# Kernel tuning notes

Hardware: AMD Instinct MI355X
Metric: run time of the kernel (lower is better)

The kernel has to match this reference:

```python
import jax, jax.numpy as jnp
import numpy as np

N = 50000
E = 400000
IN_NODE = 256
IN_EATTR = 64
IN_ETYPE = 64
EMB_EATTR = 128
EMB_ETYPE = 128
EMB_NODE = 128
OUT = 128
HEADS = 8
N_NODE_TYPES = 3
SLOPE = 0.2


def _lrelu(x):
    return jnp.where(x >= 0, x, SLOPE * x)


def setup_inputs() -> dict:
    key = jax.random.key(0)
    ks = jax.random.split(key, 12)
    s = lambda fan_in: 1.0 / np.sqrt(fan_in)
    return {
        "node_feats": jax.random.normal(ks[0], (N, IN_NODE), dtype=jnp.float32),
        "edge_index": jax.random.randint(ks[1], (2, E), 0, N, dtype=jnp.int64),
        "edge_attr": jax.random.normal(ks[2], (E, IN_EATTR), dtype=jnp.float32),
        "edge_type": jax.random.normal(ks[3], (E, IN_ETYPE), dtype=jnp.float32),
        "node_type_list": jax.random.randint(ks[4], (N,), 0, N_NODE_TYPES, dtype=jnp.int64),
        "edge_type_list": jax.random.randint(ks[5], (E,), 0, 4, dtype=jnp.int64),
        # one Linear per node type, stacked: [T, in, emb]
        "W_node": jax.random.uniform(ks[6], (N_NODE_TYPES, IN_NODE, EMB_NODE), jnp.float32, -s(IN_NODE), s(IN_NODE)),
        "W_eattr": jax.random.uniform(ks[7], (IN_EATTR, EMB_EATTR), jnp.float32, -s(IN_EATTR), s(IN_EATTR)),
        "W_etype": jax.random.uniform(ks[8], (IN_ETYPE, EMB_ETYPE), jnp.float32, -s(IN_ETYPE), s(IN_ETYPE)),
        "W_upd": jax.random.uniform(ks[9], (EMB_NODE + EMB_EATTR, OUT), jnp.float32, -s(EMB_NODE + EMB_EATTR), s(EMB_NODE + EMB_EATTR)),
        "W_attn": jax.random.uniform(ks[10], (EMB_EATTR + EMB_ETYPE + 2 * EMB_NODE, HEADS), jnp.float32, -s(512), s(512)),
    }


def reference(node_feats, edge_index, edge_attr, edge_type, node_type_list,
              edge_type_list, W_node, W_eattr, W_etype, W_upd, W_attn):
    # type-specific node embedding: project with all type weights, select per node
    all_emb = jnp.einsum("ni,tio->tno", node_feats, W_node)            # [T, N, emb]
    node_emb = jnp.take_along_axis(all_emb, node_type_list[None, :, None], axis=0)[0]  # [N, emb]

    attr_emb = _lrelu(edge_attr @ W_eattr)                             # [E, emb_a]
    type_emb = _lrelu(edge_type @ W_etype)                             # [E, emb_t]

    src, tar = edge_index[0], edge_index[1]
    src_emb = node_emb[src]                                            # [E, emb]
    tar_emb = node_emb[tar]                                            # [E, emb]

    # cat(tar_emb, attr_emb, type_emb, src_emb) -> attention scores per edge
    feat = jnp.concatenate([tar_emb, attr_emb, type_emb, src_emb], axis=1)
    scores = _lrelu(feat @ W_attn)                                     # [E, H]

    # segment softmax over edges grouped by SOURCE node (torch softmax(dim=1)
    # on the dense [src, tar, H] matrix; -10000 fillers underflow to 0)
    seg_max = jax.ops.segment_max(scores, src, num_segments=N)         # [N, H]
    ex = jnp.exp(scores - seg_max[src])
    denom = jax.ops.segment_sum(ex, src, num_segments=N)               # [N, H]
    attn = ex / denom[src]                                             # [E, H]

    msg = _lrelu(jnp.concatenate([src_emb, attr_emb], axis=1) @ W_upd) # [E, O]
    out = jax.ops.segment_sum(attn[:, :, None] * msg[:, None, :], src, num_segments=N)  # [N, H, O]
    return out.reshape(N, HEADS * OUT)
```

## Files before the change

kernel.cpp:

```cpp
#include <hip/hip_runtime.h>
#include <hip/hip_bf16.h>

#define N_NODES 50000
#define N_EDGES 400000
#define SLOPE 0.2f

typedef __attribute__((ext_vector_type(8))) short bf16x8;
typedef __attribute__((ext_vector_type(4))) float f32x4;
#define MFMA_BF16 __builtin_amdgcn_mfma_f32_16x16x32_bf16

static __device__ __forceinline__ float lrelu(float x) { return x >= 0.f ? x : SLOPE * x; }
static __device__ __forceinline__ float b2f(__hip_bfloat16 x) { return __bfloat162float(x); }
static __device__ __forceinline__ float u2f(unsigned short u) {
    union { unsigned short u; __hip_bfloat16 b; } cv; cv.u = u; return __bfloat162float(cv.b);
}
static __device__ __forceinline__ unsigned short f2bf(float x) {
    union { __hip_bfloat16 b; unsigned short u; } cv; cv.b = __float2bfloat16(x); return cv.u;
}
static __device__ __forceinline__ int clampi(int v, int lo, int hi) {
    return v < lo ? lo : (v > hi ? hi : v);
}
static __device__ __forceinline__ float ldF(const void* __restrict__ p, size_t i, bool isb) {
    return isb ? b2f(((const __hip_bfloat16*)p)[i]) : ((const float*)p)[i];
}
static __device__ __forceinline__ int ldI(const void* __restrict__ p, size_t i, bool i64) {
    return i64 ? (int)(((const long long*)p)[i]) : ((const int*)p)[i];
}

__global__ void k_detect(const void* __restrict__ nf, const void* __restrict__ eidx,
                         int* __restrict__ flags)
{
    int t = threadIdx.x;
    float x = b2f(((const __hip_bfloat16*)nf)[2 * t]);
    bool bad = !(x == x) || fabsf(x) > 1e4f;
    unsigned long long fmask = __ballot(bad);
    int v = ((const int*)eidx)[2 * t + 1];
    unsigned long long imask = __ballot(v != 0);
    if (t == 0) {
        flags[0] = (fmask == 0ull) ? 1 : 0;
        flags[1] = (imask == 0ull) ? 1 : 0;
    }
}

__global__ __launch_bounds__(256) void k_wprep(
    const void* __restrict__ Wn, const void* __restrict__ Wea, const void* __restrict__ Wet,
    const void* __restrict__ Wup, const void* __restrict__ Wat,
    unsigned short* __restrict__ WnT, unsigned short* __restrict__ WeaT,
    unsigned short* __restrict__ WetT, unsigned short* __restrict__ Wu1T,
    unsigned short* __restrict__ Wu2T, unsigned short* __restrict__ WatMidT,
    unsigned short* __restrict__ WatTS, const int* __restrict__ flags)
{
    const bool isb = flags[0] != 0;
    int i = blockIdx.x * 256 + threadIdx.x;
    if (i < 3 * 128 * 256) {
        int ty = i >> 15, rem = i & 32767, c = rem >> 8, k = rem & 255;
        WnT[i] = f2bf(ldF(Wn, ((size_t)ty * 256 + k) * 128 + c, isb));
    }
    if (i < 128 * 128) {
        int c = i >> 7, k = i & 127;
        Wu1T[i] = f2bf(ldF(Wup, (size_t)k * 128 + c, isb));
        Wu2T[i] = f2bf(ldF(Wup, (size_t)(128 + k) * 128 + c, isb));
    }
    if (i < 128 * 64) {
        int c = i >> 6, k = i & 63;
        WeaT[i] = f2bf(ldF(Wea, (size_t)k * 128 + c, isb));
        WetT[i] = f2bf(ldF(Wet, (size_t)k * 128 + c, isb));
    }
    if (i < 16 * 256) {
        int c = i >> 8, k = i & 255;
        WatMidT[i] = (c < 8) ? f2bf(ldF(Wat, (size_t)(128 + k) * 8 + c, isb)) : (unsigned short)0;
    }
    if (i < 16 * 128) {
        int c = i >> 7, k = i & 127;
        WatTS[i] = (c < 8) ? f2bf(ldF(Wat, (size_t)k * 8 + c, isb))
                           : f2bf(ldF(Wat, (size_t)(384 + k) * 8 + (c - 8), isb));
    }
}

__global__ __launch_bounds__(256) void k_node(
    const void* __restrict__ nf, const void* __restrict__ ntype,
    const unsigned short* __restrict__ WnT, const unsigned short* __restrict__ Wu1T,
    const unsigned short* __restrict__ WatTS,
    unsigned short* __restrict__ base, float* __restrict__ c_ts,
    const int* __restrict__ flags)
{
    const bool isb = flags[0] != 0, i64 = flags[1] != 0;
    const int t = threadIdx.x, lane = t & 63, wid = t >> 6;
    const int m = wid & 1, nh = wid >> 1;
    const int lr = lane & 15, lg = lane >> 4;
    const int n0 = blockIdx.x * 32;

    __shared__ __align__(16) unsigned short s_x[32 * 264];
    __shared__ __align__(16) unsigned short s_emb[32 * 136];
    __shared__ int s_ty[32];

    if (t < 32) {
        int nn = n0 + t;
        s_ty[t] = clampi(ldI(ntype, nn < N_NODES ? nn : N_NODES - 1, i64), 0, 2);
    }
    if (isb) {
        for (int i = t; i < 32 * 32; i += 256) {
            int r = i >> 5, c8 = (i & 31) * 8;
            bf16x8 v = (bf16x8)(short)0;
            if (n0 + r < N_NODES)
                v = *(const bf16x8*)((const unsigned short*)nf + (size_t)(n0 + r) * 256 + c8);
            *(bf16x8*)&s_x[r * 264 + c8] = v;
        }
    } else {
        for (int i = t; i < 32 * 64; i += 256) {
            int r = i >> 6, c4 = (i & 63) * 4;
            float4 v = make_float4(0.f, 0.f, 0.f, 0.f);
            if (n0 + r < N_NODES)
                v = *(const float4*)((const float*)nf + (size_t)(n0 + r) * 256 + c4);
            unsigned short* d = &s_x[r * 264 + c4];
            d[0] = f2bf(v.x); d[1] = f2bf(v.y); d[2] = f2bf(v.z); d[3] = f2bf(v.w);
        }
    }
    __syncthreads();

    bf16x8 A[8];
    #pragma unroll
    for (int ks = 0; ks < 8; ++ks)
        A[ks] = *(const bf16x8*)&s_x[(m * 16 + lr) * 264 + ks * 32 + lg * 8];

    f32x4 acc0[4], acc1[4], acc2[4];
    #pragma unroll
    for (int ct = 0; ct < 4; ++ct) {
        acc0[ct] = (f32x4)(0.f); acc1[ct] = (f32x4)(0.f); acc2[ct] = (f32x4)(0.f);
    }
    #pragma unroll
    for (int ct = 0; ct < 4; ++ct) {
        const int crow = nh * 64 + ct * 16 + lr;
        #pragma unroll
        for (int ks = 0; ks < 8; ++ks) {
            const int koff = ks * 32 + lg * 8;
            bf16x8 B0 = *(const bf16x8*)(WnT + (size_t)crow * 256 + koff);
            bf16x8 B1 = *(const bf16x8*)(WnT + (size_t)(128 + crow) * 256 + koff);
            bf16x8 B2 = *(const bf16x8*)(WnT + (size_t)(256 + crow) * 256 + koff);
            acc0[ct] = MFMA_BF16(A[ks], B0, acc0[ct], 0, 0, 0);
            acc1[ct] = MFMA_BF16(A[ks], B1, acc1[ct], 0, 0, 0);
            acc2[ct] = MFMA_BF16(A[ks], B2, acc2[ct], 0, 0, 0);
        }
    }
    #pragma unroll
    for (int ct = 0; ct < 4; ++ct) {
        const int col = nh * 64 + ct * 16 + lr;
        #pragma unroll
        for (int j = 0; j < 4; ++j) {
            const int row = m * 16 + lg * 4 + j;
            int ty = s_ty[row];
            float v = (ty == 0) ? acc0[ct][j] : ((ty == 1) ? acc1[ct][j] : acc2[ct][j]);
            s_emb[row * 136 + col] = f2bf(v);
        }
    }
    __syncthreads();

    bf16x8 A2[4];
    #pragma unroll
    for (int ks = 0; ks < 4; ++ks)
        A2[ks] = *(const bf16x8*)&s_emb[(m * 16 + lr) * 136 + ks * 32 + lg * 8];

    f32x4 accB[4];
    #pragma unroll
    for (int ct = 0; ct < 4; ++ct) accB[ct] = (f32x4)(0.f);
    #pragma unroll
    for (int ct = 0; ct < 4; ++ct) {
        const int crow = nh * 64 + ct * 16 + lr;
        #pragma unroll
        for (int ks = 0; ks < 4; ++ks) {
            bf16x8 B = *(const bf16x8*)(Wu1T + (size_t)crow * 128 + ks * 32 + lg * 8);
            accB[ct] = MFMA_BF16(A2[ks], B, accB[ct], 0, 0, 0);
        }
    }
    #pragma unroll
    for (int ct = 0; ct < 4; ++ct) {
        const int col = nh * 64 + ct * 16 + lr;
        #pragma unroll
        for (int j = 0; j < 4; ++j) {
            const int n = n0 + m * 16 + lg * 4 + j;
            if (n < N_NODES) base[(size_t)n * 128 + col] = f2bf(accB[ct][j]);
        }
    }

    if (nh == 0) {
        f32x4 aS = (f32x4)(0.f);
        #pragma unroll
        for (int ks = 0; ks < 4; ++ks) {
            bf16x8 B = *(const bf16x8*)(WatTS + (size_t)lr * 128 + ks * 32 + lg * 8);
            aS = MFMA_BF16(A2[ks], B, aS, 0, 0, 0);
        }
        #pragma unroll
        for (int j = 0; j < 4; ++j) {
            const int n = n0 + m * 16 + lg * 4 + j;
            if (n < N_NODES) c_ts[(size_t)n * 16 + lr] = aS[j];
        }
    }
}

__global__ __launch_bounds__(256) void k_edge(
    const void* __restrict__ eattr, const void* __restrict__ etype,
    const void* __restrict__ eidx, const float* __restrict__ c_ts,
    const unsigned short* __restrict__ WeaT, const unsigned short* __restrict__ WetT,
    const unsigned short* __restrict__ Wu2T, const unsigned short* __restrict__ WatMidT,
    float* __restrict__ scores, unsigned short* __restrict__ ap,
    const int* __restrict__ flags)
{
    const bool isb = flags[0] != 0, i64 = flags[1] != 0;
    const int t = threadIdx.x, lane = t & 63, m = t >> 6;
    const int lr = lane & 15, lg = lane >> 4;
    const int e0 = blockIdx.x * 64;

    __shared__ int s_idx[128];
    __shared__ float s_cs[64 * 16];
    __shared__ __align__(16) unsigned short s_ae[64 * 136];
    __shared__ __align__(16) unsigned short s_te[64 * 136];

    if (t < 128) {
        int e = e0 + (t & 63);
        int v = (t < 64) ? ldI(eidx, (size_t)e, i64)
                         : ldI(eidx, (size_t)N_EDGES + e, i64);
        s_idx[t] = clampi(v, 0, N_NODES - 1);
    }
    __syncthreads();
    for (int i = t; i < 1024; i += 256) {
        int e = i >> 4, c = i & 15;
        int node = (c < 8) ? s_idx[64 + e] : s_idx[e];
        s_cs[i] = c_ts[(size_t)node * 16 + c];
    }

    const int arow = e0 + m * 16 + lr;
    bf16x8 Aea[2], Aet[2];
    #pragma unroll
    for (int ks = 0; ks < 2; ++ks) {
        const int koff = ks * 32 + lg * 8;
        if (isb) {
            Aea[ks] = *(const bf16x8*)((const unsigned short*)eattr + (size_t)arow * 64 + koff);
            Aet[ks] = *(const bf16x8*)((const unsigned short*)etype + (size_t)arow * 64 + koff);
        } else {
            const float* pa = (const float*)eattr + (size_t)arow * 64 + koff;
            const float* pt = (const float*)etype + (size_t)arow * 64 + koff;
            float4 a0 = *(const float4*)pa, a1 = *(const float4*)(pa + 4);
            float4 t0 = *(const float4*)pt, t1 = *(const float4*)(pt + 4);
            bf16x8 va, vt;
            va[0] = (short)f2bf(a0.x); va[1] = (short)f2bf(a0.y);
            va[2] = (short)f2bf(a0.z); va[3] = (short)f2bf(a0.w);
            va[4] = (short)f2bf(a1.x); va[5] = (short)f2bf(a1.y);
            va[6] = (short)f2bf(a1.z); va[7] = (short)f2bf(a1.w);
            vt[0] = (short)f2bf(t0.x); vt[1] = (short)f2bf(t0.y);
            vt[2] = (short)f2bf(t0.z); vt[3] = (short)f2bf(t0.w);
            vt[4] = (short)f2bf(t1.x); vt[5] = (short)f2bf(t1.y);
            vt[6] = (short)f2bf(t1.z); vt[7] = (short)f2bf(t1.w);
            Aea[ks] = va; Aet[ks] = vt;
        }
    }
    #pragma unroll
    for (int half = 0; half < 2; ++half) {
        f32x4 aa[4], ab[4];
        #pragma unroll
        for (int ct = 0; ct < 4; ++ct) { aa[ct] = (f32x4)(0.f); ab[ct] = (f32x4)(0.f); }
        #pragma unroll
        for (int ct = 0; ct < 4; ++ct) {
            const int crow = half * 64 + ct * 16 + lr;
            #pragma unroll
            for (int ks = 0; ks < 2; ++ks) {
                const int koff = ks * 32 + lg * 8;
                bf16x8 Bea = *(const bf16x8*)(WeaT + (size_t)crow * 64 + koff);
                bf16x8 Bet = *(const bf16x8*)(WetT + (size_t)crow * 64 + koff);
                aa[ct] = MFMA_BF16(Aea[ks], Bea, aa[ct], 0, 0, 0);
                ab[ct] = MFMA_BF16(Aet[ks], Bet, ab[ct], 0, 0, 0);
            }
        }
        #pragma unroll
        for (int ct = 0; ct < 4; ++ct) {
            const int col = half * 64 + ct * 16 + lr;
            #pragma unroll
            for (int j = 0; j < 4; ++j) {
                const int row = m * 16 + lg * 4 + j;
                s_ae[row * 136 + col] = f2bf(lrelu(aa[ct][j]));
                s_te[row * 136 + col] = f2bf(lrelu(ab[ct][j]));
            }
        }
    }
    __syncthreads();

    bf16x8 A2[4];
    #pragma unroll
    for (int ks = 0; ks < 4; ++ks)
        A2[ks] = *(const bf16x8*)&s_ae[(m * 16 + lr) * 136 + ks * 32 + lg * 8];
    #pragma unroll
    for (int half = 0; half < 2; ++half) {
        f32x4 a2[4];
        #pragma unroll
        for (int ct = 0; ct < 4; ++ct) a2[ct] = (f32x4)(0.f);
        #pragma unroll
        for (int ct = 0; ct < 4; ++ct) {
            const int crow = half * 64 + ct * 16 + lr;
            #pragma unroll
            for (int ks = 0; ks < 4; ++ks) {
                bf16x8 B = *(const bf16x8*)(Wu2T + (size_t)crow * 128 + ks * 32 + lg * 8);
                a2[ct] = MFMA_BF16(A2[ks], B, a2[ct], 0, 0, 0);
            }
        }
        #pragma unroll
        for (int ct = 0; ct < 4; ++ct) {
            const int col = half * 64 + ct * 16 + lr;
            #pragma unroll
            for (int j = 0; j < 4; ++j) {
                const int e = e0 + m * 16 + lg * 4 + j;
                ap[(size_t)e * 128 + col] = f2bf(a2[ct][j]);
            }
        }
    }

    f32x4 aS = (f32x4)(0.f);
    #pragma unroll
    for (int ks = 0; ks < 8; ++ks) {
        const int koff = (ks & 3) * 32 + lg * 8;
        bf16x8 Af = (ks < 4) ? A2[ks]
                  : *(const bf16x8*)&s_te[(m * 16 + lr) * 136 + koff];
        bf16x8 B = *(const bf16x8*)(WatMidT + (size_t)lr * 256 + ks * 32 + lg * 8);
        aS = MFMA_BF16(Af, B, aS, 0, 0, 0);
    }
    if (lr < 8) {
        #pragma unroll
        for (int j = 0; j < 4; ++j) {
            const int row = m * 16 + lg * 4 + j;
            const int e = e0 + row;
            float v = aS[j] + s_cs[row * 16 + lr] + s_cs[row * 16 + 8 + lr];
            scores[(size_t)e * 8 + lr] = lrelu(v);
        }
    }
}

__global__ void k_hist(const void* __restrict__ eidx, int* __restrict__ counts,
                       const int* __restrict__ flags)
{
    const bool i64 = flags[1] != 0;
    int e = blockIdx.x * blockDim.x + threadIdx.x;
    if (e < N_EDGES) atomicAdd(&counts[clampi(ldI(eidx, e, i64), 0, N_NODES - 1)], 1);
}

__global__ __launch_bounds__(256) void k_scan1(const int* __restrict__ counts,
                                               int* __restrict__ offsets, int* __restrict__ bsum)
{
    __shared__ int buf[256];
    int b = blockIdx.x, t = threadIdx.x, i = b * 256 + t;
    int v = (i < N_NODES) ? counts[i] : 0;
    buf[t] = v;
    __syncthreads();
    for (int d = 1; d < 256; d <<= 1) {
        int add = (t >= d) ? buf[t - d] : 0;
        __syncthreads();
        buf[t] += add;
        __syncthreads();
    }
    if (i < N_NODES) offsets[i] = buf[t] - v;
    if (t == 255) bsum[b] = buf[255];
}
__global__ __launch_bounds__(256) void k_scan2(int* __restrict__ bsum, int nb)
{
    __shared__ int buf[256];
    int t = threadIdx.x;
    int v = (t < nb) ? bsum[t] : 0;
    buf[t] = v;
    __syncthreads();
    for (int d = 1; d < 256; d <<= 1) {
        int add = (t >= d) ? buf[t - d] : 0;
        __syncthreads();
        buf[t] += add;
        __syncthreads();
    }
    if (t < nb) bsum[t] = buf[t] - v;
}
__global__ __launch_bounds__(256) void k_scan3(int* __restrict__ offsets,
                                               const int* __restrict__ bsum)
{
    int i = blockIdx.x * 256 + threadIdx.x;
    if (i < N_NODES) offsets[i] += bsum[i >> 8];
    if (i == 0) offsets[N_NODES] = N_EDGES;
}

__global__ void k_scatter(const void* __restrict__ eidx, const int* __restrict__ offsets,
                          int* __restrict__ fill, int* __restrict__ perm,
                          const int* __restrict__ flags)
{
    const bool i64 = flags[1] != 0;
    int e = blockIdx.x * blockDim.x + threadIdx.x;
    if (e >= N_EDGES) return;
    int s = clampi(ldI(eidx, e, i64), 0, N_NODES - 1);
    int p = atomicAdd(&fill[s], 1);
    perm[offsets[s] + p] = e;
}

__global__ void k_stats(float* __restrict__ scores, const int* __restrict__ offsets,
                        const int* __restrict__ perm)
{
    int tid = blockIdx.x * blockDim.x + threadIdx.x;
    if (tid >= N_NODES * 8) return;
    int n = tid >> 3, h = tid & 7;
    int off = offsets[n], deg = offsets[n + 1] - off;
    if (deg <= 0) return;
    float m = -1e30f;
    for (int j = 0; j < deg; ++j) {
        int e = clampi(perm[off + j], 0, N_EDGES - 1);
        m = fmaxf(m, scores[(size_t)e * 8 + h]);
    }
    float d = 0.f;
    for (int j = 0; j < deg; ++j) {
        int e = clampi(perm[off + j], 0, N_EDGES - 1);
        d += expf(scores[(size_t)e * 8 + h] - m);
    }
    float inv = (d > 0.f) ? 1.f / d : 0.f;
    for (int j = 0; j < deg; ++j) {
        int e = clampi(perm[off + j], 0, N_EDGES - 1);
        scores[(size_t)e * 8 + h] = expf(scores[(size_t)e * 8 + h] - m) * inv;
    }
}

__global__ __launch_bounds__(128) void k_aggr2(
    const unsigned short* __restrict__ base, const float* __restrict__ attn,
    const unsigned short* __restrict__ ap, const int* __restrict__ offsets,
    const int* __restrict__ perm, void* __restrict__ out, const int* __restrict__ flags)
{
    const bool isb = flags[0] != 0;
    int n = blockIdx.x, t = threadIdx.x;
    float basev = u2f(base[(size_t)n * 128 + t]);
    float acc[8];
    #pragma unroll
    for (int h = 0; h < 8; ++h) acc[h] = 0.f;
    int off = offsets[n], deg = offsets[n + 1] - off;
    for (int j = 0; j < deg; ++j) {
        int e = clampi(perm[off + j], 0, N_EDGES - 1);
        float msg = lrelu(basev + u2f(ap[(size_t)e * 128 + t]));
        const float* at = attn + (size_t)e * 8;
        #pragma unroll
        for (int h = 0; h < 8; ++h) acc[h] += at[h] * msg;
    }
    if (isb) {
        __hip_bfloat16* o = (__hip_bfloat16*)out;
        #pragma unroll
        for (int h = 0; h < 8; ++h)
            o[(size_t)n * 1024 + h * 128 + t] = __float2bfloat16(acc[h]);
    } else {
        float* o = (float*)out;
        #pragma unroll
        for (int h = 0; h < 8; ++h)
            o[(size_t)n * 1024 + h * 128 + t] = acc[h];
    }
}

static inline size_t alignup(size_t x, size_t a) { return (x + a - 1) & ~(a - 1); }

extern "C" void kernel_launch(void* const* d_in, const int* in_sizes, int n_in,
                              void* d_out, int out_size, void* d_ws, size_t ws_size,
                              hipStream_t stream)
{
    const void* nf   = d_in[0];
    const void* eidx = d_in[1];
    const void* eatt = d_in[2];
    const void* etyp = d_in[3];
    const void* ntyp = d_in[4];
    const void* Wn   = d_in[6];
    const void* Wea  = d_in[7];
    const void* Wet  = d_in[8];
    const void* Wup  = d_in[9];
    const void* Wat  = d_in[10];

    char* w = (char*)d_ws;
    size_t off = 16;
    int* flags = (int*)w;
    unsigned short* base = (unsigned short*)(w + off);  off += (size_t)N_NODES * 128 * 2;
    float* c_ts   = (float*)(w + off);                  off += (size_t)N_NODES * 16 * 4;
    float* scores = (float*)(w + off);                  off += (size_t)N_EDGES * 8 * 4;
    int* counts   = (int*)(w + off);                    off += (size_t)N_NODES * 4;
    int* offsets  = (int*)(w + off);                    off += (size_t)(N_NODES + 1) * 4;
    int* perm     = (int*)(w + off);                    off += (size_t)N_EDGES * 4;
    int* bsum     = (int*)(w + off);                    off += 1024;
    off = alignup(off, 16);
    unsigned short* WnT     = (unsigned short*)(w + off); off += (size_t)3 * 128 * 256 * 2;
    unsigned short* WeaT    = (unsigned short*)(w + off); off += 128 * 64 * 2;
    unsigned short* WetT    = (unsigned short*)(w + off); off += 128 * 64 * 2;
    unsigned short* Wu1T    = (unsigned short*)(w + off); off += 128 * 128 * 2;
    unsigned short* Wu2T    = (unsigned short*)(w + off); off += 128 * 128 * 2;
    unsigned short* WatMidT = (unsigned short*)(w + off); off += 16 * 256 * 2;
    unsigned short* WatTS   = (unsigned short*)(w + off); off += 16 * 128 * 2;
    off = alignup(off, 16);
    unsigned short* ap = (unsigned short*)(w + off);

    hipMemsetAsync(counts, 0, N_NODES * sizeof(int), stream);

    k_detect<<<1, 64, 0, stream>>>(nf, eidx, flags);
    k_wprep<<<384, 256, 0, stream>>>(Wn, Wea, Wet, Wup, Wat,
                                     WnT, WeaT, WetT, Wu1T, Wu2T, WatMidT, WatTS, flags);
    k_node<<<(N_NODES + 31) / 32, 256, 0, stream>>>(nf, ntyp, WnT, Wu1T, WatTS,
                                                    base, c_ts, flags);
    k_edge<<<N_EDGES / 64, 256, 0, stream>>>(eatt, etyp, eidx, c_ts,
                                             WeaT, WetT, Wu2T, WatMidT, scores, ap, flags);
    k_hist<<<(N_EDGES + 255) / 256, 256, 0, stream>>>(eidx, counts, flags);
    const int SB = (N_NODES + 255) / 256;
    k_scan1<<<SB, 256, 0, stream>>>(counts, offsets, bsum);
    k_scan2<<<1, 256, 0, stream>>>(bsum, SB);
    k_scan3<<<SB, 256, 0, stream>>>(offsets, bsum);
    hipMemsetAsync(counts, 0, N_NODES * sizeof(int), stream);
    k_scatter<<<(N_EDGES + 255) / 256, 256, 0, stream>>>(eidx, offsets, counts, perm, flags);
    k_stats<<<(N_NODES * 8 + 255) / 256, 256, 0, stream>>>(scores, offsets, perm);
    k_aggr2<<<N_NODES, 128, 0, stream>>>(base, scores, ap, offsets, perm, d_out, flags);
}
```

Baseline: 903.7 us.

## Write edge scores and messages directly into CSR-sorted slots

Edges are now bucketed by source before the edge kernel runs. The scatter kernel stores each edge's destination slot (`inv`) instead of a permutation, and the edge kernel writes scores and `ap` rows straight into source-sorted positions. This lets k_stats and k_aggr2 read contiguous rows with no dependent perm lookups. The edge kernel also shrinks to 32 edges per 128-thread block and reuses a single LDS buffer, staging `ap` rows so each is written with 16-byte stores; the cost is that its global writes now land at scattered positions.

```diff
diff --git a/kernel.cpp b/kernel.cpp
--- a/kernel.cpp
+++ b/kernel.cpp
@@ -197,96 +197,127 @@
     }
 }
 
-__global__ __launch_bounds__(256) void k_edge(
+static __device__ __forceinline__ void load_afrag64(
+    bf16x8 Af[2], const void* __restrict__ src, int arow, int lg, bool isb)
+{
+    #pragma unroll
+    for (int ks = 0; ks < 2; ++ks) {
+        const int koff = ks * 32 + lg * 8;
+        if (isb) {
+            Af[ks] = *(const bf16x8*)((const unsigned short*)src + (size_t)arow * 64 + koff);
+        } else {
+            const float* p = (const float*)src + (size_t)arow * 64 + koff;
+            float4 a0 = *(const float4*)p, a1 = *(const float4*)(p + 4);
+            bf16x8 v;
+            v[0] = (short)f2bf(a0.x); v[1] = (short)f2bf(a0.y);
+            v[2] = (short)f2bf(a0.z); v[3] = (short)f2bf(a0.w);
+            v[4] = (short)f2bf(a1.x); v[5] = (short)f2bf(a1.y);
+            v[6] = (short)f2bf(a1.z); v[7] = (short)f2bf(a1.w);
+            Af[ks] = v;
+        }
+    }
+}
+
+static __device__ __forceinline__ void proj64_to_lds(
+    const bf16x8 Af[2], const unsigned short* __restrict__ WT,
+    unsigned short* __restrict__ s_buf, int m, int lr, int lg)
+{
+    #pragma unroll
+    for (int half = 0; half < 2; ++half) {
+        f32x4 acc[4];
+        #pragma unroll
+        for (int ct = 0; ct < 4; ++ct) acc[ct] = (f32x4)(0.f);
+        #pragma unroll
+        for (int ct = 0; ct < 4; ++ct) {
+            const int crow = half * 64 + ct * 16 + lr;
+            #pragma unroll
+            for (int ks = 0; ks < 2; ++ks) {
+                bf16x8 B = *(const bf16x8*)(WT + (size_t)crow * 64 + ks * 32 + lg * 8);
+                acc[ct] = MFMA_BF16(Af[ks], B, acc[ct], 0, 0, 0);
+            }
+        }
+        #pragma unroll
+        for (int ct = 0; ct < 4; ++ct) {
+            const int col = half * 64 + ct * 16 + lr;
+            #pragma unroll
+            for (int j = 0; j < 4; ++j)
+                s_buf[(m * 16 + lg * 4 + j) * 132 + col] = f2bf(lrelu(acc[ct][j]));
+        }
+    }
+}
+
+__global__ __launch_bounds__(128) void k_edge(
     const void* __restrict__ eattr, const void* __restrict__ etype,
     const void* __restrict__ eidx, const float* __restrict__ c_ts,
     const unsigned short* __restrict__ WeaT, const unsigned short* __restrict__ WetT,
     const unsigned short* __restrict__ Wu2T, const unsigned short* __restrict__ WatMidT,
-    float* __restrict__ scores, unsigned short* __restrict__ ap,
-    const int* __restrict__ flags)
+    const int* __restrict__ inv, float* __restrict__ scores,
+    unsigned short* __restrict__ ap, const int* __restrict__ flags)
 {
     const bool isb = flags[0] != 0, i64 = flags[1] != 0;
     const int t = threadIdx.x, lane = t & 63, m = t >> 6;
     const int lr = lane & 15, lg = lane >> 4;
-    const int e0 = blockIdx.x * 64;
-
-    __shared__ int s_idx[128];
-    __shared__ float s_cs[64 * 16];
-    __shared__ __align__(16) unsigned short s_ae[64 * 136];
-    __shared__ __align__(16) unsigned short s_te[64 * 136];
-
-    if (t < 128) {
-        int e = e0 + (t & 63);
-        int v = (t < 64) ? ldI(eidx, (size_t)e, i64)
+    const int e0 = blockIdx.x * 32;
+
+    __shared__ int s_idx[64];
+    __shared__ int s_slot[32];
+    __shared__ float s_cs[32 * 16];
+    __shared__ __align__(16) unsigned short s_buf[32 * 132];
+
+    if (t < 64) {
+        int e = e0 + (t & 31);
+        int v = (t < 32) ? ldI(eidx, (size_t)e, i64)
                          : ldI(eidx, (size_t)N_EDGES + e, i64);
         s_idx[t] = clampi(v, 0, N_NODES - 1);
     }
-    __syncthreads();
-    for (int i = t; i < 1024; i += 256) {
+    if (t < 32) s_slot[t] = clampi(inv[e0 + t], 0, N_EDGES - 1);
+    __syncthreads();
+
+    for (int i = t; i < 512; i += 128) {
         int e = i >> 4, c = i & 15;
-        int node = (c < 8) ? s_idx[64 + e] : s_idx[e];
+        int node = (c < 8) ? s_idx[32 + e] : s_idx[e];
         s_cs[i] = c_ts[(size_t)node * 16 + c];
     }
 
     const int arow = e0 + m * 16 + lr;
-    bf16x8 Aea[2], Aet[2];
-    #pragma unroll
-    for (int ks = 0; ks < 2; ++ks) {
-        const int koff = ks * 32 + lg * 8;
-        if (isb) {
-            Aea[ks] = *(const bf16x8*)((const unsigned short*)eattr + (size_t)arow * 64 + koff);
-            Aet[ks] = *(const bf16x8*)((const unsigned short*)etype + (size_t)arow * 64 + koff);
-        } else {
-            const float* pa = (const float*)eattr + (size_t)arow * 64 + koff;
-            const float* pt = (const float*)etype + (size_t)arow * 64 + koff;
-            float4 a0 = *(const float4*)pa, a1 = *(const float4*)(pa + 4);
-            float4 t0 = *(const float4*)pt, t1 = *(const float4*)(pt + 4);
-            bf16x8 va, vt;
-            va[0] = (short)f2bf(a0.x); va[1] = (short)f2bf(a0.y);
-            va[2] = (short)f2bf(a0.z); va[3] = (short)f2bf(a0.w);
-            va[4] = (short)f2bf(a1.x); va[5] = (short)f2bf(a1.y);
-            va[6] = (short)f2bf(a1.z); va[7] = (short)f2bf(a1.w);
-            vt[0] = (short)f2bf(t0.x); vt[1] = (short)f2bf(t0.y);
-            vt[2] = (short)f2bf(t0.z); vt[3] = (short)f2bf(t0.w);
-            vt[4] = (short)f2bf(t1.x); vt[5] = (short)f2bf(t1.y);
-            vt[6] = (short)f2bf(t1.z); vt[7] = (short)f2bf(t1.w);
-            Aea[ks] = va; Aet[ks] = vt;
-        }
-    }
-    #pragma unroll
-    for (int half = 0; half < 2; ++half) {
-        f32x4 aa[4], ab[4];
-        #pragma unroll
-        for (int ct = 0; ct < 4; ++ct) { aa[ct] = (f32x4)(0.f); ab[ct] = (f32x4)(0.f); }
-        #pragma unroll
-        for (int ct = 0; ct < 4; ++ct) {
-            const int crow = half * 64 + ct * 16 + lr;
-            #pragma unroll
-            for (int ks = 0; ks < 2; ++ks) {
-                const int koff = ks * 32 + lg * 8;
-                bf16x8 Bea = *(const bf16x8*)(WeaT + (size_t)crow * 64 + koff);
-                bf16x8 Bet = *(const bf16x8*)(WetT + (size_t)crow * 64 + koff);
-                aa[ct] = MFMA_BF16(Aea[ks], Bea, aa[ct], 0, 0, 0);
-                ab[ct] = MFMA_BF16(Aet[ks], Bet, ab[ct], 0, 0, 0);
-            }
-        }
-        #pragma unroll
-        for (int ct = 0; ct < 4; ++ct) {
-            const int col = half * 64 + ct * 16 + lr;
-            #pragma unroll
-            for (int j = 0; j < 4; ++j) {
-                const int row = m * 16 + lg * 4 + j;
-                s_ae[row * 136 + col] = f2bf(lrelu(aa[ct][j]));
-                s_te[row * 136 + col] = f2bf(lrelu(ab[ct][j]));
-            }
-        }
-    }
-    __syncthreads();
-
+    f32x4 aS = (f32x4)(0.f);
+
+    {
+        bf16x8 Aet[2];
+        load_afrag64(Aet, etype, arow, lg, isb);
+        proj64_to_lds(Aet, WetT, s_buf, m, lr, lg);
+    }
+    #pragma unroll
+    for (int ks = 0; ks < 4; ++ks) {
+        bf16x8 A = *(const bf16x8*)&s_buf[(m * 16 + lr) * 132 + ks * 32 + lg * 8];
+        bf16x8 B = *(const bf16x8*)(WatMidT + (size_t)lr * 256 + 128 + ks * 32 + lg * 8);
+        aS = MFMA_BF16(A, B, aS, 0, 0, 0);
+    }
+    {
+        bf16x8 Aea[2];
+        load_afrag64(Aea, eattr, arow, lg, isb);
+        proj64_to_lds(Aea, WeaT, s_buf, m, lr, lg);
+    }
     bf16x8 A2[4];
     #pragma unroll
     for (int ks = 0; ks < 4; ++ks)
-        A2[ks] = *(const bf16x8*)&s_ae[(m * 16 + lr) * 136 + ks * 32 + lg * 8];
+        A2[ks] = *(const bf16x8*)&s_buf[(m * 16 + lr) * 132 + ks * 32 + lg * 8];
+    #pragma unroll
+    for (int ks = 0; ks < 4; ++ks) {
+        bf16x8 B = *(const bf16x8*)(WatMidT + (size_t)lr * 256 + ks * 32 + lg * 8);
+        aS = MFMA_BF16(A2[ks], B, aS, 0, 0, 0);
+    }
+    __syncthreads();
+
+    if (lr < 8) {
+        #pragma unroll
+        for (int j = 0; j < 4; ++j) {
+            const int row = m * 16 + lg * 4 + j;
+            float v = aS[j] + s_cs[row * 16 + lr] + s_cs[row * 16 + 8 + lr];
+            scores[(size_t)s_slot[row] * 8 + lr] = lrelu(v);
+        }
+    }
+
     #pragma unroll
     for (int half = 0; half < 2; ++half) {
         f32x4 a2[4];
@@ -305,30 +336,18 @@
         for (int ct = 0; ct < 4; ++ct) {
             const int col = half * 64 + ct * 16 + lr;
             #pragma unroll
-            for (int j = 0; j < 4; ++j) {
-                const int e = e0 + m * 16 + lg * 4 + j;
-                ap[(size_t)e * 128 + col] = f2bf(a2[ct][j]);
-            }
-        }
-    }
-
-    f32x4 aS = (f32x4)(0.f);
-    #pragma unroll
-    for (int ks = 0; ks < 8; ++ks) {
-        const int koff = (ks & 3) * 32 + lg * 8;
-        bf16x8 Af = (ks < 4) ? A2[ks]
-                  : *(const bf16x8*)&s_te[(m * 16 + lr) * 136 + koff];
-        bf16x8 B = *(const bf16x8*)(WatMidT + (size_t)lr * 256 + ks * 32 + lg * 8);
-        aS = MFMA_BF16(Af, B, aS, 0, 0, 0);
-    }
-    if (lr < 8) {
-        #pragma unroll
-        for (int j = 0; j < 4; ++j) {
-            const int row = m * 16 + lg * 4 + j;
-            const int e = e0 + row;
-            float v = aS[j] + s_cs[row * 16 + lr] + s_cs[row * 16 + 8 + lr];
-            scores[(size_t)e * 8 + lr] = lrelu(v);
-        }
+            for (int j = 0; j < 4; ++j)
+                s_buf[(m * 16 + lg * 4 + j) * 132 + col] = f2bf(a2[ct][j]);
+        }
+    }
+    __syncthreads();
+
+    #pragma unroll
+    for (int i = 0; i < 4; ++i) {
+        int r = (t >> 4) + i * 8;
+        int c8 = (t & 15) * 8;
+        bf16x8 v = *(const bf16x8*)&s_buf[r * 132 + c8];
+        *(bf16x8*)(ap + (size_t)s_slot[r] * 128 + c8) = v;
     }
 }
 
@@ -381,7 +400,7 @@
 }
 
 __global__ void k_scatter(const void* __restrict__ eidx, const int* __restrict__ offsets,
-                          int* __restrict__ fill, int* __restrict__ perm,
+                          int* __restrict__ fill, int* __restrict__ inv,
                           const int* __restrict__ flags)
 {
     const bool i64 = flags[1] != 0;
@@ -389,11 +408,10 @@
     if (e >= N_EDGES) return;
     int s = clampi(ldI(eidx, e, i64), 0, N_NODES - 1);
     int p = atomicAdd(&fill[s], 1);
-    perm[offsets[s] + p] = e;
-}
-
-__global__ void k_stats(float* __restrict__ scores, const int* __restrict__ offsets,
-                        const int* __restrict__ perm)
+    inv[e] = offsets[s] + p;
+}
+
+__global__ void k_stats(float* __restrict__ scores, const int* __restrict__ offsets)
 {
     int tid = blockIdx.x * blockDim.x + threadIdx.x;
     if (tid >= N_NODES * 8) return;
@@ -401,26 +419,22 @@
     int off = offsets[n], deg = offsets[n + 1] - off;
     if (deg <= 0) return;
     float m = -1e30f;
-    for (int j = 0; j < deg; ++j) {
-        int e = clampi(perm[off + j], 0, N_EDGES - 1);
-        m = fmaxf(m, scores[(size_t)e * 8 + h]);
-    }
+    for (int j = 0; j < deg; ++j)
+        m = fmaxf(m, scores[(size_t)(off + j) * 8 + h]);
     float d = 0.f;
-    for (int j = 0; j < deg; ++j) {
-        int e = clampi(perm[off + j], 0, N_EDGES - 1);
-        d += expf(scores[(size_t)e * 8 + h] - m);
-    }
+    for (int j = 0; j < deg; ++j)
+        d += expf(scores[(size_t)(off + j) * 8 + h] - m);
     float inv = (d > 0.f) ? 1.f / d : 0.f;
     for (int j = 0; j < deg; ++j) {
-        int e = clampi(perm[off + j], 0, N_EDGES - 1);
-        scores[(size_t)e * 8 + h] = expf(scores[(size_t)e * 8 + h] - m) * inv;
+        size_t idx = (size_t)(off + j) * 8 + h;
+        scores[idx] = expf(scores[idx] - m) * inv;
     }
 }
 
 __global__ __launch_bounds__(128) void k_aggr2(
     const unsigned short* __restrict__ base, const float* __restrict__ attn,
     const unsigned short* __restrict__ ap, const int* __restrict__ offsets,
-    const int* __restrict__ perm, void* __restrict__ out, const int* __restrict__ flags)
+    void* __restrict__ out, const int* __restrict__ flags)
 {
     const bool isb = flags[0] != 0;
     int n = blockIdx.x, t = threadIdx.x;
@@ -430,9 +444,9 @@
     for (int h = 0; h < 8; ++h) acc[h] = 0.f;
     int off = offsets[n], deg = offsets[n + 1] - off;
     for (int j = 0; j < deg; ++j) {
-        int e = clampi(perm[off + j], 0, N_EDGES - 1);
-        float msg = lrelu(basev + u2f(ap[(size_t)e * 128 + t]));
-        const float* at = attn + (size_t)e * 8;
+        size_t slot = (size_t)(off + j);
+        float msg = lrelu(basev + u2f(ap[slot * 128 + t]));
+        const float* at = attn + slot * 8;
         #pragma unroll
         for (int h = 0; h < 8; ++h) acc[h] += at[h] * msg;
     }
@@ -474,7 +488,7 @@
     float* scores = (float*)(w + off);                  off += (size_t)N_EDGES * 8 * 4;
     int* counts   = (int*)(w + off);                    off += (size_t)N_NODES * 4;
     int* offsets  = (int*)(w + off);                    off += (size_t)(N_NODES + 1) * 4;
-    int* perm     = (int*)(w + off);                    off += (size_t)N_EDGES * 4;
+    int* inv      = (int*)(w + off);                    off += (size_t)N_EDGES * 4;
     int* bsum     = (int*)(w + off);                    off += 1024;
     off = alignup(off, 16);
     unsigned short* WnT     = (unsigned short*)(w + off); off += (size_t)3 * 128 * 256 * 2;
@@ -492,17 +506,19 @@
     k_detect<<<1, 64, 0, stream>>>(nf, eidx, flags);
     k_wprep<<<384, 256, 0, stream>>>(Wn, Wea, Wet, Wup, Wat,
                                      WnT, WeaT, WetT, Wu1T, Wu2T, WatMidT, WatTS, flags);
-    k_node<<<(N_NODES + 31) / 32, 256, 0, stream>>>(nf, ntyp, WnT, Wu1T, WatTS,
-                                                    base, c_ts, flags);
-    k_edge<<<N_EDGES / 64, 256, 0, stream>>>(eatt, etyp, eidx, c_ts,
-                                             WeaT, WetT, Wu2T, WatMidT, scores, ap, flags);
     k_hist<<<(N_EDGES + 255) / 256, 256, 0, stream>>>(eidx, counts, flags);
     const int SB = (N_NODES + 255) / 256;
     k_scan1<<<SB, 256, 0, stream>>>(counts, offsets, bsum);
     k_scan2<<<1, 256, 0, stream>>>(bsum, SB);
     k_scan3<<<SB, 256, 0, stream>>>(offsets, bsum);
     hipMemsetAsync(counts, 0, N_NODES * sizeof(int), stream);
-    k_scatter<<<(N_EDGES + 255) / 256, 256, 0, stream>>>(eidx, offsets, counts, perm, flags);
-    k_stats<<<(N_NODES * 8 + 255) / 256, 256, 0, stream>>>(scores, offsets, perm);
-    k_aggr2<<<N_NODES, 128, 0, stream>>>(base, scores, ap, offsets, perm, d_out, flags);
-}
+    k_scatter<<<(N_EDGES + 255) / 256, 256, 0, stream>>>(eidx, offsets, counts, inv, flags);
+
+    k_node<<<(N_NODES + 31) / 32, 256, 0, stream>>>(nf, ntyp, WnT, Wu1T, WatTS,
+                                                    base, c_ts, flags);
+    k_edge<<<N_EDGES / 32, 128, 0, stream>>>(eatt, etyp, eidx, c_ts,
+                                             WeaT, WetT, Wu2T, WatMidT,
+                                             inv, scores, ap, flags);
+    k_stats<<<(N_NODES * 8 + 255) / 256, 256, 0, stream>>>(scores, offsets);
+    k_aggr2<<<N_NODES, 128, 0, stream>>>(base, scores, ap, offsets, d_out, flags);
+}
```

Measured after the change: 829.0 us. 8.3% less time.
